# Optimization experiments

Measured on AMD Instinct MI355X. Metric: run time of the kernel, lower is better.

Reference implementation:

```python
import jax, jax.numpy as jnp
import numpy as np

D = 10          # tree depth (perfect binary tree, heap layout)
K = 2           # MAX_CHILD
N = 2 ** D - 1  # nodes per tree = 1023
LD = 256        # latent_dim
B = 128         # batch of trees


def setup_inputs() -> dict:
    key = jax.random.key(0)
    ks = jax.random.split(key, 24)
    p = lambda k, shape: (jax.random.normal(k, shape, jnp.float32) * 0.05)
    return {
        "x_embed": jax.random.normal(ks[0], (B, N, LD), jnp.float32),
        "init_embedding": jax.random.normal(ks[1], (B, LD), jnp.float32),
        # leaf gates cx, ox
        "Wcx": p(ks[2], (LD, LD)), "bcx": p(ks[3], (LD,)),
        "Wox": p(ks[4], (LD, LD)), "box": p(ks[5], (LD,)),
        # token-input gates ix, fx, ux
        "Wix": p(ks[6], (LD, LD)), "bix": p(ks[7], (LD,)),
        "Wfx": p(ks[8], (LD, LD)), "bfx": p(ks[9], (LD,)),
        "Wux": p(ks[10], (LD, LD)), "bux": p(ks[11], (LD,)),
        # per-child gates: i_gates[K], f_gates[K][K], u_gates[K]
        "Wi": p(ks[12], (K, LD, LD)), "bi": p(ks[13], (K, LD)),
        "Wf": p(ks[14], (K, K, LD, LD)), "bf": p(ks[15], (K, K, LD)),
        "Wu": p(ks[16], (K, LD, LD)), "bu": p(ks[17], (K, LD)),
        # output projection oend: Linear(3*latent_dim, latent_dim)
        "Woend": p(ks[18], (3 * LD, LD)), "boend": p(ks[19], (LD,)),
    }


def _tree_lstm(x_embed, Wcx, bcx, Wox, box, Wix, bix, Wfx, bfx, Wux, bux,
               Wi, bi, Wf, bf, Wu, bu):
    lin = lambda x, W, b: x @ W + b
    # --- leaves (deepest level): c = cx(x); h = sigmoid(ox(x)) * tanh(c) ---
    leaf_start = 2 ** (D - 1) - 1
    x_leaf = x_embed[:, leaf_start:]                       # [B, 2^(D-1), d]
    c_leaf = lin(x_leaf, Wcx, bcx)
    h_leaf = jax.nn.sigmoid(lin(x_leaf, Wox, box)) * jnp.tanh(c_leaf)
    c_all = jnp.zeros_like(x_embed).at[:, leaf_start:].set(c_leaf)
    h_all = jnp.zeros_like(x_embed).at[:, leaf_start:].set(h_leaf)
    # --- internal levels, bottom-up (fixed D-1 iterations, vectorized over B*width) ---
    for lvl in range(D - 2, -1, -1):
        s, e = 2 ** lvl - 1, 2 ** (lvl + 1) - 1
        idx = np.arange(s, e)
        ch = np.stack([2 * idx + 1, 2 * idx + 2], axis=1)  # [w, K] heap children
        hch = h_all[:, ch]                                 # [B, w, K, d]
        cch = c_all[:, ch]                                 # [B, w, K, d]
        x = x_embed[:, s:e]                                # [B, w, d]
        # i = sigmoid(ix(x) + sum_k i_gates[k](h_k))
        i = jax.nn.sigmoid(lin(x, Wix, bix)
                           + jnp.einsum('bwkd,kde->bwe', hch, Wi) + bi.sum(0))
        # f_vals[k] = fx(x) + sum_j f_gates[k][j](h_j)   (NO sigmoid, faithful to source)
        f = (lin(x, Wfx, bfx)[:, :, None, :]
             + jnp.einsum('bwjd,kjde->bwke', hch, Wf) + bf.sum(1))   # [B, w, K, d]
        # u = tanh(ux(x) + sum_k u_gates[k](h_k))
        u = jnp.tanh(lin(x, Wux, bux)
                     + jnp.einsum('bwkd,kde->bwe', hch, Wu) + bu.sum(0))
        c = i * u + jnp.sum(f * cch, axis=2)
        h = jnp.tanh(c)
        c_all = c_all.at[:, s:e].set(c)
        h_all = h_all.at[:, s:e].set(h)
    return c_all[:, 0], h_all[:, 0]                        # root state (c, h)


def reference(x_embed, init_embedding, Wcx, bcx, Wox, box, Wix, bix, Wfx, bfx,
              Wux, bux, Wi, bi, Wf, bf, Wu, bu, Woend, boend):
    c_root, h_root = _tree_lstm(x_embed, Wcx, bcx, Wox, box, Wix, bix,
                                Wfx, bfx, Wux, bux, Wi, bi, Wf, bf, Wu, bu)
    s = jnp.concatenate([init_embedding, c_root, h_root], axis=1)  # [B, 3d]
    return jnp.tanh(s @ Woend + boend)                             # [B, d]
```

## Files before the change

### kernel.cpp

```cpp
#include <hip/hip_runtime.h>
#include <hip/hip_bf16.h>
#include <math.h>


#define NNODES 1023
#define BATCH  128
#define LDIM   256

typedef __attribute__((ext_vector_type(8))) short short8;
typedef __attribute__((ext_vector_type(4))) float f32x4;

__device__ __forceinline__ float sigmoidf_(float x) {
    return 1.f / (1.f + expf(-x));
}

__device__ __forceinline__ void split3(float x, ushort& h, ushort& m, ushort& l) {
    unsigned u = __float_as_uint(x);
    unsigned hu = (u + 0x7FFFu + ((u >> 16) & 1u)) & 0xFFFF0000u;
    h = (ushort)(hu >> 16);
    float r = x - __uint_as_float(hu);
    unsigned ur = __float_as_uint(r);
    unsigned mu = (ur + 0x7FFFu + ((ur >> 16) & 1u)) & 0xFFFF0000u;
    m = (ushort)(mu >> 16);
    float r2 = r - __uint_as_float(mu);
    unsigned u2 = __float_as_uint(r2);
    l = (ushort)((u2 + 0x7FFFu + ((u2 >> 16) & 1u)) >> 16);
}

__device__ __forceinline__ unsigned cvt_pk_bf16(float lo, float hi) {
    unsigned r;
    asm("v_cvt_pk_bf16_f32 %0, %1, %2" : "=v"(r) : "v"(lo), "v"(hi));
    return r;
}

struct P3 { unsigned h, m, l; };
__device__ __forceinline__ P3 pack2v(float x0, float x1) {
    P3 p;
    p.h = cvt_pk_bf16(x0, x1);
    float h0 = __uint_as_float(p.h << 16);
    float h1 = __uint_as_float(p.h & 0xFFFF0000u);
    float r0 = x0 - h0, r1 = x1 - h1;
    p.m = cvt_pk_bf16(r0, r1);
    float m0 = __uint_as_float(p.m << 16);
    float m1 = __uint_as_float(p.m & 0xFFFF0000u);
    p.l = cvt_pk_bf16(r0 - m0, r1 - m1);
    return p;
}

struct VF { short8 h, m, l; };
__device__ __forceinline__ VF split8(float4 a, float4 b) {
    P3 p0 = pack2v(a.x, a.y), p1 = pack2v(a.z, a.w);
    P3 p2 = pack2v(b.x, b.y), p3 = pack2v(b.z, b.w);
    VF r;
    r.h = __builtin_bit_cast(short8, make_uint4(p0.h, p1.h, p2.h, p3.h));
    r.m = __builtin_bit_cast(short8, make_uint4(p0.m, p1.m, p2.m, p3.m));
    r.l = __builtin_bit_cast(short8, make_uint4(p0.l, p1.l, p2.l, p3.l));
    return r;
}

__global__ __launch_bounds__(256) void build_weights(
    const float* __restrict__ Wix, const float* __restrict__ bix,
    const float* __restrict__ Wfx, const float* __restrict__ bfx,
    const float* __restrict__ Wux, const float* __restrict__ bux,
    const float* __restrict__ Wi,  const float* __restrict__ bi,
    const float* __restrict__ Wf,  const float* __restrict__ bf,
    const float* __restrict__ Wu,  const float* __restrict__ bu,
    const float* __restrict__ Wcx, const float* __restrict__ bcx,
    const float* __restrict__ Wox, const float* __restrict__ box,
    float* __restrict__ Wbig, float* __restrict__ bias_big,
    float* __restrict__ Wleaf, float* __restrict__ bias_leaf)
{
    int i = blockIdx.x * blockDim.x + threadIdx.x;
    if (i < 768 * 1024) {
        int k = i >> 10, n = i & 1023;
        int g = n >> 8, nn = n & 255;
        float v;
        if (g == 0) {
            v = (k < 256) ? Wix[k * 256 + nn]
              : (k < 512) ? Wi[(k - 256) * 256 + nn]
                          : Wi[65536 + (k - 512) * 256 + nn];
        } else if (g == 1) {
            v = (k < 256) ? Wux[k * 256 + nn]
              : (k < 512) ? Wu[(k - 256) * 256 + nn]
                          : Wu[65536 + (k - 512) * 256 + nn];
        } else {
            int kf = g - 2;
            v = (k < 256) ? Wfx[k * 256 + nn]
              : (k < 512) ? Wf[((kf * 2 + 0) * 256 + (k - 256)) * 256 + nn]
                          : Wf[((kf * 2 + 1) * 256 + (k - 512)) * 256 + nn];
        }
        Wbig[i] = v;
        return;
    }
    i -= 768 * 1024;
    if (i < 1024) {
        int g = i >> 8, nn = i & 255;
        float v;
        if (g == 0)      v = bix[nn] + bi[nn] + bi[256 + nn];
        else if (g == 1) v = bux[nn] + bu[nn] + bu[256 + nn];
        else if (g == 2) v = bfx[nn] + bf[nn] + bf[256 + nn];
        else             v = bfx[nn] + bf[512 + nn] + bf[768 + nn];
        bias_big[i] = v;
        return;
    }
    i -= 1024;
    if (i < 256 * 512) {
        int k = i >> 9, n = i & 511;
        Wleaf[i] = (n < 256) ? Wcx[k * 256 + n] : Wox[k * 256 + (n - 256)];
        return;
    }
    i -= 256 * 512;
    if (i < 512) {
        bias_leaf[i] = (i < 256) ? bcx[i] : box[i - 256];
    }
}

__global__ __launch_bounds__(256) void split_weights_T(
    const float* __restrict__ Wbig,
    ushort* __restrict__ Wth, ushort* __restrict__ Wtm, ushort* __restrict__ Wtl)
{
    __shared__ float sh[32][33];
    const int k0 = blockIdx.x * 32, n0 = blockIdx.y * 32;
    const int t = threadIdx.x;
    {
        int r = t >> 3, c4 = (t & 7) * 4;
        float4 v = *(const float4*)&Wbig[(size_t)(k0 + r) * 1024 + n0 + c4];
        sh[r][c4] = v.x; sh[r][c4 + 1] = v.y; sh[r][c4 + 2] = v.z; sh[r][c4 + 3] = v.w;
    }
    __syncthreads();
    int n = t >> 3, kc = (t & 7) * 4;
    ushort oh[4], om[4], ol[4];
#pragma unroll
    for (int j = 0; j < 4; ++j)
        split3(sh[kc + j][n], oh[j], om[j], ol[j]);
    size_t o = (size_t)(n0 + n) * 768 + k0 + kc;
    *(ushort4*)&Wth[o] = make_ushort4(oh[0], oh[1], oh[2], oh[3]);
    *(ushort4*)&Wtm[o] = make_ushort4(om[0], om[1], om[2], om[3]);
    *(ushort4*)&Wtl[o] = make_ushort4(ol[0], ol[1], ol[2], ol[3]);
}

__global__ __launch_bounds__(256) void split_wleaf_T(
    const float* __restrict__ Wleaf,
    ushort* __restrict__ Lth, ushort* __restrict__ Ltm, ushort* __restrict__ Ltl)
{
    __shared__ float sh[32][33];
    const int k0 = blockIdx.x * 32, n0 = blockIdx.y * 32;
    const int t = threadIdx.x;
    {
        int r = t >> 3, c4 = (t & 7) * 4;
        float4 v = *(const float4*)&Wleaf[(size_t)(k0 + r) * 512 + n0 + c4];
        sh[r][c4] = v.x; sh[r][c4 + 1] = v.y; sh[r][c4 + 2] = v.z; sh[r][c4 + 3] = v.w;
    }
    __syncthreads();
    int n = t >> 3, kc = (t & 7) * 4;
    ushort oh[4], om[4], ol[4];
#pragma unroll
    for (int j = 0; j < 4; ++j)
        split3(sh[kc + j][n], oh[j], om[j], ol[j]);
    size_t o = (size_t)(n0 + n) * 256 + k0 + kc;
    *(ushort4*)&Lth[o] = make_ushort4(oh[0], oh[1], oh[2], oh[3]);
    *(ushort4*)&Ltm[o] = make_ushort4(om[0], om[1], om[2], om[3]);
    *(ushort4*)&Ltl[o] = make_ushort4(ol[0], ol[1], ol[2], ol[3]);
}

__global__ __launch_bounds__(256, 3) void mfma_level_pack(
    const float* __restrict__ x_embed,
    const float* __restrict__ hChild, const float* __restrict__ cChild,
    const ushort* __restrict__ Wth, const ushort* __restrict__ Wtm,
    const ushort* __restrict__ Wtl,
    const float* __restrict__ bias,
    float* __restrict__ hOut, float* __restrict__ cOut, int nstart)
{
    __shared__ __align__(16) ushort Wlds[2][12288];

    const int tid  = threadIdx.x;
    const int node = blockIdx.x;
    const int gy   = blockIdx.y;
    const int lane = tid & 63, wid = tid >> 6;
    const int srow = tid & 127, shalf = tid >> 7;

    const size_t nb = (size_t)(((srow >> 5) << 8) + gy * 32 + (srow & 31)) * 768;
    const ushort* w0 = Wth + nb;
    const ushort* w1 = Wtm + nb;
    const ushort* w2 = Wtl + nb;

    const int b0 = wid * 32 + (lane & 15);
    const int b1 = b0 + 16;
    const int kl = (lane >> 4) * 8;
    const float* x0p = x_embed + ((size_t)b0 * NNODES + (nstart + node)) * LDIM + kl;
    const float* x1p = x_embed + ((size_t)b1 * NNODES + (nstart + node)) * LDIM + kl;
    const float* l0p = hChild + ((size_t)(2 * node) * BATCH + b0) * LDIM + kl;
    const float* l1p = hChild + ((size_t)(2 * node) * BATCH + b1) * LDIM + kl;
    const size_t RSTEP = (size_t)BATCH * LDIM;

    const int wbase = 2 * shalf * 1024 + srow * 8;
    const int rbase = (lane >> 4) * 1024 + (lane & 15) * 8;

    f32x4 acc[8][2];
#pragma unroll
    for (int ct = 0; ct < 8; ++ct)
#pragma unroll
        for (int t2 = 0; t2 < 2; ++t2) acc[ct][t2] = (f32x4){0.f, 0.f, 0.f, 0.f};

    float4 v00, v01, v10, v11;
    int4 w00, w01, w10, w11, w20, w21;

#define W_LOADS(IT)                                                            \
    {                                                                          \
        const int bko_ = (IT) * 32 + shalf * 16;                               \
        w00 = *(const int4*)(w0 + bko_); w01 = *(const int4*)(w0 + bko_ + 8);  \
        w10 = *(const int4*)(w1 + bko_); w11 = *(const int4*)(w1 + bko_ + 8);  \
        w20 = *(const int4*)(w2 + bko_); w21 = *(const int4*)(w2 + bko_ + 8);  \
    }
#define ACT_LOADS(IT)                                                          \
    {                                                                          \
        const int seg_  = (IT) >> 3;                                           \
        const int koff_ = ((IT) & 7) * 32;                                     \
        const float* pa0_ = (seg_ == 0) ? x0p : (seg_ == 1) ? l0p : (l0p + RSTEP); \
        const float* pa1_ = (seg_ == 0) ? x1p : (seg_ == 1) ? l1p : (l1p + RSTEP); \
        pa0_ += koff_; pa1_ += koff_;                                          \
        v00 = *(const float4*)(pa0_);                                          \
        v01 = *(const float4*)(pa0_ + 4);                                      \
        v10 = *(const float4*)(pa1_);                                          \
        v11 = *(const float4*)(pa1_ + 4);                                      \
    }
#define WRITE_W(BUF)                                                           \
    {                                                                          \
        ushort* wp_ = &Wlds[BUF][wbase];                                       \
        *(int4*)(wp_)        = w00; *(int4*)(wp_ + 1024) = w01;                \
        *(int4*)(wp_ + 4096) = w10; *(int4*)(wp_ + 5120) = w11;                \
        *(int4*)(wp_ + 8192) = w20; *(int4*)(wp_ + 9216) = w21;                \
    }

    W_LOADS(0); ACT_LOADS(0);
    WRITE_W(0);
    W_LOADS(1);
    __syncthreads();

    for (int it = 0; it < 24; ++it) {
        const int cur = it & 1;
        if (it + 1 < 24) WRITE_W(cur ^ 1);
        if (it + 2 < 24) W_LOADS(it + 2);
        VF f0 = split8(v00, v01);
        VF f1 = split8(v10, v11);
        if (it + 1 < 24) ACT_LOADS(it + 1);
        const ushort* lb = &Wlds[cur][rbase];
        __builtin_amdgcn_s_setprio(1);
#pragma unroll
        for (int ct = 0; ct < 8; ++ct) {
            short8 wh = *(const short8*)(lb + ct * 128);
            short8 wm = *(const short8*)(lb + 4096 + ct * 128);
            short8 wl = *(const short8*)(lb + 8192 + ct * 128);
            acc[ct][0] = __builtin_amdgcn_mfma_f32_16x16x32_bf16(wl, f0.h, acc[ct][0], 0, 0, 0);
            acc[ct][1] = __builtin_amdgcn_mfma_f32_16x16x32_bf16(wl, f1.h, acc[ct][1], 0, 0, 0);
            acc[ct][0] = __builtin_amdgcn_mfma_f32_16x16x32_bf16(wh, f0.l, acc[ct][0], 0, 0, 0);
            acc[ct][1] = __builtin_amdgcn_mfma_f32_16x16x32_bf16(wh, f1.l, acc[ct][1], 0, 0, 0);
            acc[ct][0] = __builtin_amdgcn_mfma_f32_16x16x32_bf16(wm, f0.m, acc[ct][0], 0, 0, 0);
            acc[ct][1] = __builtin_amdgcn_mfma_f32_16x16x32_bf16(wm, f1.m, acc[ct][1], 0, 0, 0);
            acc[ct][0] = __builtin_amdgcn_mfma_f32_16x16x32_bf16(wm, f0.h, acc[ct][0], 0, 0, 0);
            acc[ct][1] = __builtin_amdgcn_mfma_f32_16x16x32_bf16(wm, f1.h, acc[ct][1], 0, 0, 0);
            acc[ct][0] = __builtin_amdgcn_mfma_f32_16x16x32_bf16(wh, f0.m, acc[ct][0], 0, 0, 0);
            acc[ct][1] = __builtin_amdgcn_mfma_f32_16x16x32_bf16(wh, f1.m, acc[ct][1], 0, 0, 0);
            acc[ct][0] = __builtin_amdgcn_mfma_f32_16x16x32_bf16(wh, f0.h, acc[ct][0], 0, 0, 0);
            acc[ct][1] = __builtin_amdgcn_mfma_f32_16x16x32_bf16(wh, f1.h, acc[ct][1], 0, 0, 0);
        }
        __builtin_amdgcn_s_setprio(0);
        __syncthreads();
    }
#undef W_LOADS
#undef ACT_LOADS
#undef WRITE_W

    const size_t cLb = (size_t)(2 * node) * BATCH * LDIM;
    const size_t cRb = cLb + (size_t)BATCH * LDIM;
    const size_t ob  = (size_t)node * BATCH * LDIM;
#pragma unroll
    for (int half = 0; half < 2; ++half) {
        const int nc = gy * 32 + half * 16 + ((lane >> 4) << 2);
        const float4 bi4 = *(const float4*)&bias[nc];
        const float4 bu4 = *(const float4*)&bias[256 + nc];
        const float4 b04 = *(const float4*)&bias[512 + nc];
        const float4 b14 = *(const float4*)&bias[768 + nc];
        const float bi_[4] = {bi4.x, bi4.y, bi4.z, bi4.w};
        const float bu_[4] = {bu4.x, bu4.y, bu4.z, bu4.w};
        const float b0_[4] = {b04.x, b04.y, b04.z, b04.w};
        const float b1_[4] = {b14.x, b14.y, b14.z, b14.w};
#pragma unroll
        for (int Nt = 0; Nt < 2; ++Nt) {
            const int b = wid * 32 + Nt * 16 + (lane & 15);
            float4 cL = *(const float4*)&cChild[cLb + (size_t)b * LDIM + nc];
            float4 cR = *(const float4*)&cChild[cRb + (size_t)b * LDIM + nc];
            float cl4[4] = {cL.x, cL.y, cL.z, cL.w};
            float cr4[4] = {cR.x, cR.y, cR.z, cR.w};
            float4 c4, h4;
            float* cp = (float*)&c4; float* hp = (float*)&h4;
#pragma unroll
            for (int j = 0; j < 4; ++j) {
                float gi = sigmoidf_(acc[0 + half][Nt][j] + bi_[j]);
                float gu = tanhf(acc[2 + half][Nt][j] + bu_[j]);
                float f0 = acc[4 + half][Nt][j] + b0_[j];
                float f1 = acc[6 + half][Nt][j] + b1_[j];
                float c  = gi * gu + f0 * cl4[j] + f1 * cr4[j];
                cp[j] = c;
                hp[j] = tanhf(c);
            }
            *(float4*)&cOut[ob + (size_t)b * LDIM + nc] = c4;
            *(float4*)&hOut[ob + (size_t)b * LDIM + nc] = h4;
        }
    }
}

__global__ __launch_bounds__(256, 3) void leaf_mfma(
    const float* __restrict__ x_embed,
    const ushort* __restrict__ Lth, const ushort* __restrict__ Ltm,
    const ushort* __restrict__ Ltl,
    const float* __restrict__ bias_leaf,
    float* __restrict__ hOut, float* __restrict__ cOut)
{
    constexpr int AST = 40;
    __shared__ __align__(16) ushort Wlds[3][64 * AST];
    __shared__ __align__(16) ushort Vlds[3][128 * AST];

    const int tid = threadIdx.x;
    const int ln  = blockIdx.x;
    const int gy  = blockIdx.y;
    const int lane = tid & 63, wid = tid >> 6;
    const int ni = wid & 1, bw = wid >> 1;
    const int srow = tid & 127, shalf = tid >> 7;
    const int wrow = tid & 63, whalf = (tid >> 6) & 1;

    const float* aX = x_embed + ((size_t)srow * NNODES + (511 + ln)) * LDIM;
    const size_t nbw = (size_t)(((wrow >> 5) << 8) + gy * 32 + (wrow & 31)) * 256;
    const ushort* l0 = Lth + nbw;
    const ushort* l1 = Ltm + nbw;
    const ushort* l2 = Ltl + nbw;

    f32x4 acc[2][4];
#pragma unroll
    for (int g = 0; g < 2; ++g)
#pragma unroll
        for (int t2 = 0; t2 < 4; ++t2) acc[g][t2] = (f32x4){0.f, 0.f, 0.f, 0.f};

    float4 a0, a1, a2, a3;
    int4 w00, w01, w10, w11, w20, w21;

#define LEAF_LOADS(IT)                                                         \
    {                                                                          \
        const float* ap_ = aX + (IT) * 32 + shalf * 16;                        \
        a0 = *(const float4*)(ap_);                                            \
        a1 = *(const float4*)(ap_ + 4);                                        \
        a2 = *(const float4*)(ap_ + 8);                                        \
        a3 = *(const float4*)(ap_ + 12);                                       \
        if (tid < 128) {                                                       \
            const int bko_ = (IT) * 32 + whalf * 16;                           \
            w00 = *(const int4*)(l0 + bko_); w01 = *(const int4*)(l0 + bko_ + 8); \
            w10 = *(const int4*)(l1 + bko_); w11 = *(const int4*)(l1 + bko_ + 8); \
            w20 = *(const int4*)(l2 + bko_); w21 = *(const int4*)(l2 + bko_ + 8); \
        }                                                                      \
    }

    LEAF_LOADS(0);
    for (int it = 0; it < 8; ++it) {
        if (it) __syncthreads();
        {
            P3 p0 = pack2v(a0.x, a0.y), p1 = pack2v(a0.z, a0.w);
            P3 p2 = pack2v(a1.x, a1.y), p3 = pack2v(a1.z, a1.w);
            P3 p4 = pack2v(a2.x, a2.y), p5 = pack2v(a2.z, a2.w);
            P3 p6 = pack2v(a3.x, a3.y), p7 = pack2v(a3.z, a3.w);
            const int base = srow * AST + shalf * 16;
            *(int4*)&Vlds[0][base]     = make_int4((int)p0.h, (int)p1.h, (int)p2.h, (int)p3.h);
            *(int4*)&Vlds[0][base + 8] = make_int4((int)p4.h, (int)p5.h, (int)p6.h, (int)p7.h);
            *(int4*)&Vlds[1][base]     = make_int4((int)p0.m, (int)p1.m, (int)p2.m, (int)p3.m);
            *(int4*)&Vlds[1][base + 8] = make_int4((int)p4.m, (int)p5.m, (int)p6.m, (int)p7.m);
            *(int4*)&Vlds[2][base]     = make_int4((int)p0.l, (int)p1.l, (int)p2.l, (int)p3.l);
            *(int4*)&Vlds[2][base + 8] = make_int4((int)p4.l, (int)p5.l, (int)p6.l, (int)p7.l);
            if (tid < 128) {
                const int bw_ = wrow * AST + whalf * 16;
                *(int4*)&Wlds[0][bw_]     = w00;
                *(int4*)&Wlds[0][bw_ + 8] = w01;
                *(int4*)&Wlds[1][bw_]     = w10;
                *(int4*)&Wlds[1][bw_ + 8] = w11;
                *(int4*)&Wlds[2][bw_]     = w20;
                *(int4*)&Wlds[2][bw_ + 8] = w21;
            }
        }
        __syncthreads();
        if (it + 1 < 8) LEAF_LOADS(it + 1);
        {
            short8 vf[4][3];
#pragma unroll
            for (int Nt = 0; Nt < 4; ++Nt) {
                const int rb = (bw * 64 + Nt * 16 + (lane & 15)) * AST + (lane >> 4) * 8;
#pragma unroll
                for (int s = 0; s < 3; ++s) vf[Nt][s] = *(const short8*)&Vlds[s][rb];
            }
#pragma unroll
            for (int g = 0; g < 2; ++g) {
                const int cb = (g * 32 + ni * 16 + (lane & 15)) * AST + (lane >> 4) * 8;
                short8 wh = *(const short8*)&Wlds[0][cb];
                short8 wm = *(const short8*)&Wlds[1][cb];
                short8 wl = *(const short8*)&Wlds[2][cb];
#pragma unroll
                for (int Nt = 0; Nt < 4; ++Nt)
                    acc[g][Nt] = __builtin_amdgcn_mfma_f32_16x16x32_bf16(wl, vf[Nt][0], acc[g][Nt], 0, 0, 0);
#pragma unroll
                for (int Nt = 0; Nt < 4; ++Nt)
                    acc[g][Nt] = __builtin_amdgcn_mfma_f32_16x16x32_bf16(wh, vf[Nt][2], acc[g][Nt], 0, 0, 0);
#pragma unroll
                for (int Nt = 0; Nt < 4; ++Nt)
                    acc[g][Nt] = __builtin_amdgcn_mfma_f32_16x16x32_bf16(wm, vf[Nt][1], acc[g][Nt], 0, 0, 0);
#pragma unroll
                for (int Nt = 0; Nt < 4; ++Nt)
                    acc[g][Nt] = __builtin_amdgcn_mfma_f32_16x16x32_bf16(wm, vf[Nt][0], acc[g][Nt], 0, 0, 0);
#pragma unroll
                for (int Nt = 0; Nt < 4; ++Nt)
                    acc[g][Nt] = __builtin_amdgcn_mfma_f32_16x16x32_bf16(wh, vf[Nt][1], acc[g][Nt], 0, 0, 0);
#pragma unroll
                for (int Nt = 0; Nt < 4; ++Nt)
                    acc[g][Nt] = __builtin_amdgcn_mfma_f32_16x16x32_bf16(wh, vf[Nt][0], acc[g][Nt], 0, 0, 0);
            }
        }
    }
#undef LEAF_LOADS

    const int nc = gy * 32 + ni * 16 + ((lane >> 4) << 2);
    const size_t ob = (size_t)ln * BATCH * LDIM;
    const float4 bc4 = *(const float4*)&bias_leaf[nc];
    const float4 bo4 = *(const float4*)&bias_leaf[256 + nc];
    const float bc_[4] = {bc4.x, bc4.y, bc4.z, bc4.w};
    const float bo_[4] = {bo4.x, bo4.y, bo4.z, bo4.w};
#pragma unroll
    for (int Nt = 0; Nt < 4; ++Nt) {
        const int b = bw * 64 + Nt * 16 + (lane & 15);
        float4 c4, h4;
        float* cp = (float*)&c4; float* hp = (float*)&h4;
#pragma unroll
        for (int j = 0; j < 4; ++j) {
            float c = acc[0][Nt][j] + bc_[j];
            float o = acc[1][Nt][j] + bo_[j];
            cp[j] = c;
            hp[j] = sigmoidf_(o) * tanhf(c);
        }
        size_t po = ob + (size_t)b * LDIM + nc;
        *(float4*)&cOut[po] = c4;
        *(float4*)&hOut[po] = h4;
    }
}

__global__ __launch_bounds__(256) void leaf_kernel(
    const float* __restrict__ x_embed,
    const float* __restrict__ Wleaf, const float* __restrict__ bias_leaf,
    float* __restrict__ hOut, float* __restrict__ cOut)
{
    __shared__ float As[16 * 68];
    __shared__ float Bs[2 * 16 * 64];
    float acc[2][4][4] = {};
    const int tid = threadIdx.x;
    const int ty = tid >> 4, tx = tid & 15;
    const int row0 = blockIdx.x * 64;
    const int n0 = blockIdx.y * 64;
    const int w = row0 >> 7;
    const int ar = tid >> 2;
    const int kq = (tid & 3) * 4;
    const int b = (row0 + ar) & 127;
    const float* xrow = x_embed + ((size_t)b * NNODES + 511 + w) * LDIM;

    for (int k0 = 0; k0 < 256; k0 += 16) {
        float4 av = *(const float4*)(xrow + k0 + kq);
        As[(kq + 0) * 68 + ar] = av.x;
        As[(kq + 1) * 68 + ar] = av.y;
        As[(kq + 2) * 68 + ar] = av.z;
        As[(kq + 3) * 68 + ar] = av.w;
#pragma unroll
        for (int q = 0; q < 2; ++q) {
            int L = q * 256 + tid;
            int g = L >> 8, kk = (L >> 4) & 15, n4 = (L & 15) * 4;
            float4 bv = *(const float4*)(Wleaf + (size_t)(k0 + kk) * 512 + g * 256 + n0 + n4);
            *(float4*)&Bs[(g * 16 + kk) * 64 + n4] = bv;
        }
        __syncthreads();
#pragma unroll
        for (int kk = 0; kk < 16; ++kk) {
            float4 a = *(const float4*)&As[kk * 68 + ty * 4];
            float av4[4] = {a.x, a.y, a.z, a.w};
#pragma unroll
            for (int g = 0; g < 2; ++g) {
                float4 bb = *(const float4*)&Bs[(g * 16 + kk) * 64 + tx * 4];
                float bv4[4] = {bb.x, bb.y, bb.z, bb.w};
#pragma unroll
                for (int ii = 0; ii < 4; ++ii)
#pragma unroll
                    for (int jj = 0; jj < 4; ++jj)
                        acc[g][ii][jj] += av4[ii] * bv4[jj];
            }
        }
        __syncthreads();
    }
#pragma unroll
    for (int ii = 0; ii < 4; ++ii) {
        int r = row0 + ty * 4 + ii;
        int nc = n0 + tx * 4;
        float4 c4, h4;
        float* cp = (float*)&c4; float* hp = (float*)&h4;
#pragma unroll
        for (int jj = 0; jj < 4; ++jj) {
            int n = nc + jj;
            float ac = acc[0][ii][jj] + bias_leaf[n];
            float ao = acc[1][ii][jj] + bias_leaf[256 + n];
            cp[jj] = ac;
            hp[jj] = sigmoidf_(ao) * tanhf(ac);
        }
        *(float4*)&cOut[(size_t)r * LDIM + nc] = c4;
        *(float4*)&hOut[(size_t)r * LDIM + nc] = h4;
    }
}

__global__ __launch_bounds__(256) void level_kernel(
    const float* __restrict__ x_embed,
    const float* __restrict__ hChild, const float* __restrict__ cChild,
    const float* __restrict__ Wbig, const float* __restrict__ bias_big,
    float* __restrict__ hOut, float* __restrict__ cOut,
    int nstart)
{
    __shared__ float As[16 * 68];
    __shared__ float Bs[4 * 16 * 64];
    float acc[4][4][4] = {};
    const int tid = threadIdx.x;
    const int ty = tid >> 4, tx = tid & 15;
    const int row0 = blockIdx.x * 64;
    const int n0 = blockIdx.y * 64;
    const int w = row0 >> 7;
    const int ar = tid >> 2;
    const int kq = (tid & 3) * 4;
    const int b = (row0 + ar) & 127;
    const float* srcX = x_embed + ((size_t)b * NNODES + nstart + w) * LDIM;
    const float* srcL = hChild + ((size_t)(2 * w) * BATCH + b) * LDIM;
    const float* srcR = hChild + ((size_t)(2 * w + 1) * BATCH + b) * LDIM;

    for (int k0 = 0; k0 < 768; k0 += 16) {
        int seg = k0 >> 8, off = k0 & 255;
        const float* src = (seg == 0) ? srcX : (seg == 1) ? srcL : srcR;
        float4 av = *(const float4*)(src + off + kq);
        As[(kq + 0) * 68 + ar] = av.x;
        As[(kq + 1) * 68 + ar] = av.y;
        As[(kq + 2) * 68 + ar] = av.z;
        As[(kq + 3) * 68 + ar] = av.w;
#pragma unroll
        for (int q = 0; q < 4; ++q) {
            int L = q * 256 + tid;
            int g = L >> 8, kk = (L >> 4) & 15, n4 = (L & 15) * 4;
            float4 bv = *(const float4*)(Wbig + (size_t)(k0 + kk) * 1024 + g * 256 + n0 + n4);
            *(float4*)&Bs[(g * 16 + kk) * 64 + n4] = bv;
        }
        __syncthreads();
#pragma unroll
        for (int kk = 0; kk < 16; ++kk) {
            float4 a = *(const float4*)&As[kk * 68 + ty * 4];
            float av4[4] = {a.x, a.y, a.z, a.w};
#pragma unroll
            for (int g = 0; g < 4; ++g) {
                float4 bb = *(const float4*)&Bs[(g * 16 + kk) * 64 + tx * 4];
                float bv4[4] = {bb.x, bb.y, bb.z, bb.w};
#pragma unroll
                for (int ii = 0; ii < 4; ++ii)
#pragma unroll
                    for (int jj = 0; jj < 4; ++jj)
                        acc[g][ii][jj] += av4[ii] * bv4[jj];
            }
        }
        __syncthreads();
    }
    const size_t cLbase = ((size_t)(2 * w) * BATCH) * LDIM;
    const size_t cRbase = ((size_t)(2 * w + 1) * BATCH) * LDIM;
#pragma unroll
    for (int ii = 0; ii < 4; ++ii) {
        int r = row0 + ty * 4 + ii;
        int bb2 = r & 127;
        int nc = n0 + tx * 4;
        float4 cL = *(const float4*)&cChild[cLbase + (size_t)bb2 * LDIM + nc];
        float4 cR = *(const float4*)&cChild[cRbase + (size_t)bb2 * LDIM + nc];
        float cl4[4] = {cL.x, cL.y, cL.z, cL.w};
        float cr4[4] = {cR.x, cR.y, cR.z, cR.w};
        float4 c4, h4;
        float* cp = (float*)&c4; float* hp = (float*)&h4;
#pragma unroll
        for (int jj = 0; jj < 4; ++jj) {
            int n = nc + jj;
            float gi = sigmoidf_(acc[0][ii][jj] + bias_big[n]);
            float gu = tanhf(acc[1][ii][jj] + bias_big[256 + n]);
            float f0 = acc[2][ii][jj] + bias_big[512 + n];
            float f1 = acc[3][ii][jj] + bias_big[768 + n];
            float c = gi * gu + f0 * cl4[jj] + f1 * cr4[jj];
            cp[jj] = c;
            hp[jj] = tanhf(c);
        }
        *(float4*)&cOut[(size_t)r * LDIM + nc] = c4;
        *(float4*)&hOut[(size_t)r * LDIM + nc] = h4;
    }
}

__global__ __launch_bounds__(256) void gemm_part4(
    const float* __restrict__ x_embed, const float* __restrict__ hChild,
    const float* __restrict__ Wbig,
    float* __restrict__ part, int nstart, int rowsTotal)
{
    __shared__ float As[16 * 68];
    __shared__ float Bs[4 * 16 * 64];
    float acc[4][4][4] = {};
    const int tid = threadIdx.x;
    const int ty = tid >> 4, tx = tid & 15;
    const int row0 = blockIdx.x * 64;
    const int n0 = blockIdx.y * 64;
    const int seg = blockIdx.z;
    const int w = row0 >> 7;
    const int ar = tid >> 2;
    const int kq = (tid & 3) * 4;
    const int b = (row0 + ar) & 127;
    const float* src =
        (seg == 0) ? x_embed + ((size_t)b * NNODES + nstart + w) * LDIM
                   : hChild + ((size_t)(2 * w + (seg - 1)) * BATCH + b) * LDIM;

    for (int k0 = 0; k0 < 256; k0 += 16) {
        float4 av = *(const float4*)(src + k0 + kq);
        As[(kq + 0) * 68 + ar] = av.x;
        As[(kq + 1) * 68 + ar] = av.y;
        As[(kq + 2) * 68 + ar] = av.z;
        As[(kq + 3) * 68 + ar] = av.w;
#pragma unroll
        for (int q = 0; q < 4; ++q) {
            int L = q * 256 + tid;
            int g = L >> 8, kk = (L >> 4) & 15, n4 = (L & 15) * 4;
            float4 bv = *(const float4*)(Wbig + (size_t)(seg * 256 + k0 + kk) * 1024
                                         + g * 256 + n0 + n4);
            *(float4*)&Bs[(g * 16 + kk) * 64 + n4] = bv;
        }
        __syncthreads();
#pragma unroll
        for (int kk = 0; kk < 16; ++kk) {
            float4 a = *(const float4*)&As[kk * 68 + ty * 4];
            float av4[4] = {a.x, a.y, a.z, a.w};
#pragma unroll
            for (int g = 0; g < 4; ++g) {
                float4 bb = *(const float4*)&Bs[(g * 16 + kk) * 64 + tx * 4];
                float bv4[4] = {bb.x, bb.y, bb.z, bb.w};
#pragma unroll
                for (int ii = 0; ii < 4; ++ii)
#pragma unroll
                    for (int jj = 0; jj < 4; ++jj)
                        acc[g][ii][jj] += av4[ii] * bv4[jj];
            }
        }
        __syncthreads();
    }
#pragma unroll
    for (int ii = 0; ii < 4; ++ii) {
        int r = row0 + ty * 4 + ii;
        size_t base = ((size_t)seg * rowsTotal + r) * 1024 + n0 + tx * 4;
#pragma unroll
        for (int g = 0; g < 4; ++g)
            *(float4*)&part[base + g * 256] = *(float4*)acc[g][ii];
    }
}

__global__ __launch_bounds__(256) void combine_eps(
    const float* __restrict__ part, const float* __restrict__ cChild,
    const float* __restrict__ bias,
    float* __restrict__ hOut, float* __restrict__ cOut, int rowsTotal)
{
    int idx = blockIdx.x * 256 + threadIdx.x;
    int row = idx >> 6, n = (idx & 63) * 4;
    size_t sseg = (size_t)rowsTotal * 1024;
    const float* p0 = part + (size_t)row * 1024 + n;
    float s[4][4];
#pragma unroll
    for (int g = 0; g < 4; ++g) {
        float4 a = *(const float4*)(p0 + g * 256);
        float4 b = *(const float4*)(p0 + sseg + g * 256);
        float4 c = *(const float4*)(p0 + 2 * sseg + g * 256);
        s[g][0] = a.x + b.x + c.x; s[g][1] = a.y + b.y + c.y;
        s[g][2] = a.z + b.z + c.z; s[g][3] = a.w + b.w + c.w;
    }
    int node = row >> 7, b = row & 127;
    float4 cL = *(const float4*)&cChild[((size_t)(2 * node) * BATCH + b) * LDIM + n];
    float4 cR = *(const float4*)&cChild[((size_t)(2 * node + 1) * BATCH + b) * LDIM + n];
    float cl4[4] = {cL.x, cL.y, cL.z, cL.w};
    float cr4[4] = {cR.x, cR.y, cR.z, cR.w};
    float4 c4, h4;
    float* cp = (float*)&c4; float* hp = (float*)&h4;
#pragma unroll
    for (int jj = 0; jj < 4; ++jj) {
        int nn = n + jj;
        float gi = sigmoidf_(s[0][jj] + bias[nn]);
        float gu = tanhf(s[1][jj] + bias[256 + nn]);
        float f0 = s[2][jj] + bias[512 + nn];
        float f1 = s[3][jj] + bias[768 + nn];
        float c = gi * gu + f0 * cl4[jj] + f1 * cr4[jj];
        cp[jj] = c;
        hp[jj] = tanhf(c);
    }
    *(float4*)&cOut[(size_t)row * LDIM + n] = c4;
    *(float4*)&hOut[(size_t)row * LDIM + n] = h4;
}

__global__ __launch_bounds__(256) void final_kernel(
    const float* __restrict__ init_emb,
    const float* __restrict__ cRoot, const float* __restrict__ hRoot,
    const float* __restrict__ Woend, const float* __restrict__ boend,
    float* __restrict__ out)
{
    __shared__ float sv[768];
    int b = blockIdx.x, t = threadIdx.x;
    sv[t]       = init_emb[(size_t)b * 256 + t];
    sv[256 + t] = cRoot[(size_t)b * 256 + t];
    sv[512 + t] = hRoot[(size_t)b * 256 + t];
    __syncthreads();
    float acc = boend[t];
#pragma unroll 4
    for (int d = 0; d < 768; ++d)
        acc += sv[d] * Woend[(size_t)d * 256 + t];
    out[(size_t)b * 256 + t] = tanhf(acc);
}

extern "C" void kernel_launch(void* const* d_in, const int* in_sizes, int n_in,
                              void* d_out, int out_size, void* d_ws, size_t ws_size,
                              hipStream_t stream)
{
    const float* x_embed  = (const float*)d_in[0];
    const float* init_emb = (const float*)d_in[1];
    const float* Wcx = (const float*)d_in[2];  const float* bcx = (const float*)d_in[3];
    const float* Wox = (const float*)d_in[4];  const float* box = (const float*)d_in[5];
    const float* Wix = (const float*)d_in[6];  const float* bix = (const float*)d_in[7];
    const float* Wfx = (const float*)d_in[8];  const float* bfx = (const float*)d_in[9];
    const float* Wux = (const float*)d_in[10]; const float* bux = (const float*)d_in[11];
    const float* Wi  = (const float*)d_in[12]; const float* bi  = (const float*)d_in[13];
    const float* Wf  = (const float*)d_in[14]; const float* bf  = (const float*)d_in[15];
    const float* Wu  = (const float*)d_in[16]; const float* bu  = (const float*)d_in[17];
    const float* Woend = (const float*)d_in[18]; const float* boend = (const float*)d_in[19];
    float* out = (float*)d_out;
    float* ws  = (float*)d_ws;

    size_t off = 0;
    float* hA = ws + off; off += (size_t)512 * 128 * 256;
    float* cA = ws + off; off += (size_t)512 * 128 * 256;
    float* hB = ws + off; off += (size_t)256 * 128 * 256;
    float* cB = ws + off; off += (size_t)256 * 128 * 256;
    float* Wbig      = ws + off; off += (size_t)768 * 1024;
    float* bias_big  = ws + off; off += 1024;
    float* Wleaf     = ws + off; off += (size_t)256 * 512;
    float* bias_leaf = ws + off; off += 512;
    ushort* Wth = (ushort*)(ws + off); off += (size_t)768 * 1024 / 2;
    ushort* Wtm = (ushort*)(ws + off); off += (size_t)768 * 1024 / 2;
    ushort* Wtl = (ushort*)(ws + off); off += (size_t)768 * 1024 / 2;
    ushort* Lth = (ushort*)(ws + off); off += (size_t)512 * 256 / 2;
    ushort* Ltm = (ushort*)(ws + off); off += (size_t)512 * 256 / 2;
    ushort* Ltl = (ushort*)(ws + off); off += (size_t)512 * 256 / 2;
    size_t mfma_need = off * sizeof(float);
    size_t part_off = off;
    float* part = ws + part_off;

    bool mfma_ok = mfma_need <= ws_size;

    {
        int total = 768 * 1024 + 1024 + 256 * 512 + 512;
        int blocks = (total + 255) / 256;
        build_weights<<<blocks, 256, 0, stream>>>(
            Wix, bix, Wfx, bfx, Wux, bux, Wi, bi, Wf, bf, Wu, bu,
            Wcx, bcx, Wox, box, Wbig, bias_big, Wleaf, bias_leaf);
    }
    if (mfma_ok) {
        split_weights_T<<<dim3(24, 32), 256, 0, stream>>>(Wbig, Wth, Wtm, Wtl);
        split_wleaf_T<<<dim3(8, 16), 256, 0, stream>>>(Wleaf, Lth, Ltm, Ltl);
    }

    if (mfma_ok) {
        leaf_mfma<<<dim3(512, 8), 256, 0, stream>>>(
            x_embed, Lth, Ltm, Ltl, bias_leaf, hA, cA);
    } else {
        leaf_kernel<<<dim3(1024, 4), 256, 0, stream>>>(
            x_embed, Wleaf, bias_leaf, hA, cA);
    }

    float* hbufs[2] = {hA, hB};
    float* cbufs[2] = {cA, cB};
    int child = 0;
    for (int lvl = 8; lvl >= 0; --lvl) {
        int W = 1 << lvl, s = W - 1;
        int outb = child ^ 1;
        size_t rows = (size_t)W * 128;
        bool split = (W <= 16) &&
                     ((part_off + 3 * rows * 1024) * sizeof(float) <= ws_size);
        if (lvl >= 5 && mfma_ok) {
            mfma_level_pack<<<dim3(W, 8), 256, 0, stream>>>(
                x_embed, hbufs[child], cbufs[child], Wth, Wtm, Wtl, bias_big,
                hbufs[outb], cbufs[outb], s);
        } else if (split) {
            gemm_part4<<<dim3(W * 2, 4, 3), 256, 0, stream>>>(
                x_embed, hbufs[child], Wbig, part, s, (int)rows);
            combine_eps<<<(int)(rows / 4), 256, 0, stream>>>(
                part, cbufs[child], bias_big, hbufs[outb], cbufs[outb], (int)rows);
        } else {
            level_kernel<<<dim3(W * 2, 4), 256, 0, stream>>>(
                x_embed, hbufs[child], cbufs[child], Wbig, bias_big,
                hbufs[outb], cbufs[outb], s);
        }
        child = outb;
    }

    final_kernel<<<128, 256, 0, stream>>>(init_emb, cbufs[child], hbufs[child],
                                          Woend, boend, out);
}
```

Before: 1.064 ms.

## Re-tile level kernel waves as 2x2 over columns and batch rows

Changes the warp-to-tile mapping in the internal-level MFMA kernel. Each wave previously covered all 128 weight columns for 32 batch rows; it now covers half the columns (one per gate pair) for 64 batch rows. This halves the per-wave LDS weight reads while doubling activation loads and split work per wave. The next activation prefetch is also moved after the MFMA block, and the epilogue is adjusted to the new ownership.

```diff
diff --git a/kernel.cpp b/kernel.cpp
--- a/kernel.cpp
+++ b/kernel.cpp
@@ -177,6 +177,7 @@
     const int node = blockIdx.x;
     const int gy   = blockIdx.y;
     const int lane = tid & 63, wid = tid >> 6;
+    const int ch = wid & 1, bh = wid >> 1;
     const int srow = tid & 127, shalf = tid >> 7;
 
     const size_t nb = (size_t)(((srow >> 5) << 8) + gy * 32 + (srow & 31)) * 768;
@@ -184,25 +185,24 @@
     const ushort* w1 = Wtm + nb;
     const ushort* w2 = Wtl + nb;
 
-    const int b0 = wid * 32 + (lane & 15);
-    const int b1 = b0 + 16;
+    const int rowb = bh * 64 + (lane & 15);
     const int kl = (lane >> 4) * 8;
-    const float* x0p = x_embed + ((size_t)b0 * NNODES + (nstart + node)) * LDIM + kl;
-    const float* x1p = x_embed + ((size_t)b1 * NNODES + (nstart + node)) * LDIM + kl;
-    const float* l0p = hChild + ((size_t)(2 * node) * BATCH + b0) * LDIM + kl;
-    const float* l1p = hChild + ((size_t)(2 * node) * BATCH + b1) * LDIM + kl;
+    const float* xb = x_embed + ((size_t)rowb * NNODES + (nstart + node)) * LDIM + kl;
+    const float* lb0 = hChild + ((size_t)(2 * node) * BATCH + rowb) * LDIM + kl;
+    const size_t XNT = (size_t)16 * NNODES * LDIM;
+    const size_t LNT = (size_t)16 * LDIM;
     const size_t RSTEP = (size_t)BATCH * LDIM;
 
     const int wbase = 2 * shalf * 1024 + srow * 8;
-    const int rbase = (lane >> 4) * 1024 + (lane & 15) * 8;
-
-    f32x4 acc[8][2];
-#pragma unroll
-    for (int ct = 0; ct < 8; ++ct)
-#pragma unroll
-        for (int t2 = 0; t2 < 2; ++t2) acc[ct][t2] = (f32x4){0.f, 0.f, 0.f, 0.f};
-
-    float4 v00, v01, v10, v11;
+    const int rbase = (lane >> 4) * 1024 + (lane & 15) * 8 + ch * 128;
+
+    f32x4 acc[4][4];
+#pragma unroll
+    for (int g = 0; g < 4; ++g)
+#pragma unroll
+        for (int t2 = 0; t2 < 4; ++t2) acc[g][t2] = (f32x4){0.f, 0.f, 0.f, 0.f};
+
+    float4 va0, vb0, va1, vb1, va2, vb2, va3, vb3;
     int4 w00, w01, w10, w11, w20, w21;
 
 #define W_LOADS(IT)                                                            \
@@ -216,13 +216,19 @@
     {                                                                          \
         const int seg_  = (IT) >> 3;                                           \
         const int koff_ = ((IT) & 7) * 32;                                     \
-        const float* pa0_ = (seg_ == 0) ? x0p : (seg_ == 1) ? l0p : (l0p + RSTEP); \
-        const float* pa1_ = (seg_ == 0) ? x1p : (seg_ == 1) ? l1p : (l1p + RSTEP); \
-        pa0_ += koff_; pa1_ += koff_;                                          \
-        v00 = *(const float4*)(pa0_);                                          \
-        v01 = *(const float4*)(pa0_ + 4);                                      \
-        v10 = *(const float4*)(pa1_);                                          \
-        v11 = *(const float4*)(pa1_ + 4);                                      \
+        if (seg_ == 0) {                                                       \
+            const float* p_ = xb + koff_;                                      \
+            va0 = *(const float4*)(p_);             vb0 = *(const float4*)(p_ + 4); \
+            va1 = *(const float4*)(p_ + XNT);       vb1 = *(const float4*)(p_ + XNT + 4); \
+            va2 = *(const float4*)(p_ + 2 * XNT);   vb2 = *(const float4*)(p_ + 2 * XNT + 4); \
+            va3 = *(const float4*)(p_ + 3 * XNT);   vb3 = *(const float4*)(p_ + 3 * XNT + 4); \
+        } else {                                                               \
+            const float* p_ = lb0 + ((seg_ == 2) ? RSTEP : 0) + koff_;         \
+            va0 = *(const float4*)(p_);             vb0 = *(const float4*)(p_ + 4); \
+            va1 = *(const float4*)(p_ + LNT);       vb1 = *(const float4*)(p_ + LNT + 4); \
+            va2 = *(const float4*)(p_ + 2 * LNT);   vb2 = *(const float4*)(p_ + 2 * LNT + 4); \
+            va3 = *(const float4*)(p_ + 3 * LNT);   vb3 = *(const float4*)(p_ + 3 * LNT + 4); \
+        }                                                                      \
     }
 #define WRITE_W(BUF)                                                           \
     {                                                                          \
@@ -241,30 +247,45 @@
         const int cur = it & 1;
         if (it + 1 < 24) WRITE_W(cur ^ 1);
         if (it + 2 < 24) W_LOADS(it + 2);
-        VF f0 = split8(v00, v01);
-        VF f1 = split8(v10, v11);
+        VF f0 = split8(va0, vb0);
+        VF f1 = split8(va1, vb1);
+        VF f2 = split8(va2, vb2);
+        VF f3 = split8(va3, vb3);
+        const ushort* lp = &Wlds[cur][rbase];
+        __builtin_amdgcn_s_setprio(1);
+#pragma unroll
+        for (int g = 0; g < 4; ++g) {
+            const int off = g * 256;
+            short8 wh = *(const short8*)(lp + off);
+            short8 wm = *(const short8*)(lp + 4096 + off);
+            short8 wl = *(const short8*)(lp + 8192 + off);
+            acc[g][0] = __builtin_amdgcn_mfma_f32_16x16x32_bf16(wl, f0.h, acc[g][0], 0, 0, 0);
+            acc[g][1] = __builtin_amdgcn_mfma_f32_16x16x32_bf16(wl, f1.h, acc[g][1], 0, 0, 0);
+            acc[g][2] = __builtin_amdgcn_mfma_f32_16x16x32_bf16(wl, f2.h, acc[g][2], 0, 0, 0);
+            acc[g][3] = __builtin_amdgcn_mfma_f32_16x16x32_bf16(wl, f3.h, acc[g][3], 0, 0, 0);
+            acc[g][0] = __builtin_amdgcn_mfma_f32_16x16x32_bf16(wh, f0.l, acc[g][0], 0, 0, 0);
+            acc[g][1] = __builtin_amdgcn_mfma_f32_16x16x32_bf16(wh, f1.l, acc[g][1], 0, 0, 0);
+            acc[g][2] = __builtin_amdgcn_mfma_f32_16x16x32_bf16(wh, f2.l, acc[g][2], 0, 0, 0);
+            acc[g][3] = __builtin_amdgcn_mfma_f32_16x16x32_bf16(wh, f3.l, acc[g][3], 0, 0, 0);
+            acc[g][0] = __builtin_amdgcn_mfma_f32_16x16x32_bf16(wm, f0.m, acc[g][0], 0, 0, 0);
+            acc[g][1] = __builtin_amdgcn_mfma_f32_16x16x32_bf16(wm, f1.m, acc[g][1], 0, 0, 0);
+            acc[g][2] = __builtin_amdgcn_mfma_f32_16x16x32_bf16(wm, f2.m, acc[g][2], 0, 0, 0);
+            acc[g][3] = __builtin_amdgcn_mfma_f32_16x16x32_bf16(wm, f3.m, acc[g][3], 0, 0, 0);
+            acc[g][0] = __builtin_amdgcn_mfma_f32_16x16x32_bf16(wm, f0.h, acc[g][0], 0, 0, 0);
+            acc[g][1] = __builtin_amdgcn_mfma_f32_16x16x32_bf16(wm, f1.h, acc[g][1], 0, 0, 0);
+            acc[g][2] = __builtin_amdgcn_mfma_f32_16x16x32_bf16(wm, f2.h, acc[g][2], 0, 0, 0);
+            acc[g][3] = __builtin_amdgcn_mfma_f32_16x16x32_bf16(wm, f3.h, acc[g][3], 0, 0, 0);
+            acc[g][0] = __builtin_amdgcn_mfma_f32_16x16x32_bf16(wh, f0.m, acc[g][0], 0, 0, 0);
+            acc[g][1] = __builtin_amdgcn_mfma_f32_16x16x32_bf16(wh, f1.m, acc[g][1], 0, 0, 0);
+            acc[g][2] = __builtin_amdgcn_mfma_f32_16x16x32_bf16(wh, f2.m, acc[g][2], 0, 0, 0);
+            acc[g][3] = __builtin_amdgcn_mfma_f32_16x16x32_bf16(wh, f3.m, acc[g][3], 0, 0, 0);
+            acc[g][0] = __builtin_amdgcn_mfma_f32_16x16x32_bf16(wh, f0.h, acc[g][0], 0, 0, 0);
+            acc[g][1] = __builtin_amdgcn_mfma_f32_16x16x32_bf16(wh, f1.h, acc[g][1], 0, 0, 0);
+            acc[g][2] = __builtin_amdgcn_mfma_f32_16x16x32_bf16(wh, f2.h, acc[g][2], 0, 0, 0);
+            acc[g][3] = __builtin_amdgcn_mfma_f32_16x16x32_bf16(wh, f3.h, acc[g][3], 0, 0, 0);
+        }
+        __builtin_amdgcn_s_setprio(0);
         if (it + 1 < 24) ACT_LOADS(it + 1);
-        const ushort* lb = &Wlds[cur][rbase];
-        __builtin_amdgcn_s_setprio(1);
-#pragma unroll
-        for (int ct = 0; ct < 8; ++ct) {
-            short8 wh = *(const short8*)(lb + ct * 128);
-            short8 wm = *(const short8*)(lb + 4096 + ct * 128);
-            short8 wl = *(const short8*)(lb + 8192 + ct * 128);
-            acc[ct][0] = __builtin_amdgcn_mfma_f32_16x16x32_bf16(wl, f0.h, acc[ct][0], 0, 0, 0);
-            acc[ct][1] = __builtin_amdgcn_mfma_f32_16x16x32_bf16(wl, f1.h, acc[ct][1], 0, 0, 0);
-            acc[ct][0] = __builtin_amdgcn_mfma_f32_16x16x32_bf16(wh, f0.l, acc[ct][0], 0, 0, 0);
-            acc[ct][1] = __builtin_amdgcn_mfma_f32_16x16x32_bf16(wh, f1.l, acc[ct][1], 0, 0, 0);
-            acc[ct][0] = __builtin_amdgcn_mfma_f32_16x16x32_bf16(wm, f0.m, acc[ct][0], 0, 0, 0);
-            acc[ct][1] = __builtin_amdgcn_mfma_f32_16x16x32_bf16(wm, f1.m, acc[ct][1], 0, 0, 0);
-            acc[ct][0] = __builtin_amdgcn_mfma_f32_16x16x32_bf16(wm, f0.h, acc[ct][0], 0, 0, 0);
-            acc[ct][1] = __builtin_amdgcn_mfma_f32_16x16x32_bf16(wm, f1.h, acc[ct][1], 0, 0, 0);
-            acc[ct][0] = __builtin_amdgcn_mfma_f32_16x16x32_bf16(wh, f0.m, acc[ct][0], 0, 0, 0);
-            acc[ct][1] = __builtin_amdgcn_mfma_f32_16x16x32_bf16(wh, f1.m, acc[ct][1], 0, 0, 0);
-            acc[ct][0] = __builtin_amdgcn_mfma_f32_16x16x32_bf16(wh, f0.h, acc[ct][0], 0, 0, 0);
-            acc[ct][1] = __builtin_amdgcn_mfma_f32_16x16x32_bf16(wh, f1.h, acc[ct][1], 0, 0, 0);
-        }
-        __builtin_amdgcn_s_setprio(0);
         __syncthreads();
     }
 #undef W_LOADS
@@ -274,39 +295,36 @@
     const size_t cLb = (size_t)(2 * node) * BATCH * LDIM;
     const size_t cRb = cLb + (size_t)BATCH * LDIM;
     const size_t ob  = (size_t)node * BATCH * LDIM;
-#pragma unroll
-    for (int half = 0; half < 2; ++half) {
-        const int nc = gy * 32 + half * 16 + ((lane >> 4) << 2);
-        const float4 bi4 = *(const float4*)&bias[nc];
-        const float4 bu4 = *(const float4*)&bias[256 + nc];
-        const float4 b04 = *(const float4*)&bias[512 + nc];
-        const float4 b14 = *(const float4*)&bias[768 + nc];
-        const float bi_[4] = {bi4.x, bi4.y, bi4.z, bi4.w};
-        const float bu_[4] = {bu4.x, bu4.y, bu4.z, bu4.w};
-        const float b0_[4] = {b04.x, b04.y, b04.z, b04.w};
-        const float b1_[4] = {b14.x, b14.y, b14.z, b14.w};
-#pragma unroll
-        for (int Nt = 0; Nt < 2; ++Nt) {
-            const int b = wid * 32 + Nt * 16 + (lane & 15);
-            float4 cL = *(const float4*)&cChild[cLb + (size_t)b * LDIM + nc];
-            float4 cR = *(const float4*)&cChild[cRb + (size_t)b * LDIM + nc];
-            float cl4[4] = {cL.x, cL.y, cL.z, cL.w};
-            float cr4[4] = {cR.x, cR.y, cR.z, cR.w};
-            float4 c4, h4;
-            float* cp = (float*)&c4; float* hp = (float*)&h4;
-#pragma unroll
-            for (int j = 0; j < 4; ++j) {
-                float gi = sigmoidf_(acc[0 + half][Nt][j] + bi_[j]);
-                float gu = tanhf(acc[2 + half][Nt][j] + bu_[j]);
-                float f0 = acc[4 + half][Nt][j] + b0_[j];
-                float f1 = acc[6 + half][Nt][j] + b1_[j];
-                float c  = gi * gu + f0 * cl4[j] + f1 * cr4[j];
-                cp[j] = c;
-                hp[j] = tanhf(c);
-            }
-            *(float4*)&cOut[ob + (size_t)b * LDIM + nc] = c4;
-            *(float4*)&hOut[ob + (size_t)b * LDIM + nc] = h4;
-        }
+    const int nc = gy * 32 + ch * 16 + ((lane >> 4) << 2);
+    const float4 bi4 = *(const float4*)&bias[nc];
+    const float4 bu4 = *(const float4*)&bias[256 + nc];
+    const float4 b04 = *(const float4*)&bias[512 + nc];
+    const float4 b14 = *(const float4*)&bias[768 + nc];
+    const float bi_[4] = {bi4.x, bi4.y, bi4.z, bi4.w};
+    const float bu_[4] = {bu4.x, bu4.y, bu4.z, bu4.w};
+    const float b0_[4] = {b04.x, b04.y, b04.z, b04.w};
+    const float b1_[4] = {b14.x, b14.y, b14.z, b14.w};
+#pragma unroll
+    for (int Nt = 0; Nt < 4; ++Nt) {
+        const int b = bh * 64 + Nt * 16 + (lane & 15);
+        float4 cL = *(const float4*)&cChild[cLb + (size_t)b * LDIM + nc];
+        float4 cR = *(const float4*)&cChild[cRb + (size_t)b * LDIM + nc];
+        float cl4[4] = {cL.x, cL.y, cL.z, cL.w};
+        float cr4[4] = {cR.x, cR.y, cR.z, cR.w};
+        float4 c4, h4;
+        float* cp = (float*)&c4; float* hp = (float*)&h4;
+#pragma unroll
+        for (int j = 0; j < 4; ++j) {
+            float gi = sigmoidf_(acc[0][Nt][j] + bi_[j]);
+            float gu = tanhf(acc[1][Nt][j] + bu_[j]);
+            float f0 = acc[2][Nt][j] + b0_[j];
+            float f1 = acc[3][Nt][j] + b1_[j];
+            float c  = gi * gu + f0 * cl4[j] + f1 * cr4[j];
+            cp[j] = c;
+            hp[j] = tanhf(c);
+        }
+        *(float4*)&cOut[ob + (size_t)b * LDIM + nc] = c4;
+        *(float4*)&hOut[ob + (size_t)b * LDIM + nc] = h4;
     }
 }
 
```

Result: slower. 1.750 ms (+64.4%).
